# Optimization experiments

Hardware: AMD Instinct MI355X
Metric: run time of the kernel (lower is better)

## Reference

```python
import jax, jax.numpy as jnp
import numpy as np

B, OBS, ACT_DIM, C, CTX, H = 128, 512, 7, 100, 128, 512
IN = OBS + 1 + CTX  # states + scalar action component + context = 641


def cont2disc(values, n):
    return jnp.clip(jnp.floor((values + 1.0) / 2.0 * n), 0, n - 1)


def setup_inputs() -> dict:
    key = jax.random.key(0)
    ks = jax.random.split(key, 10)
    def w(k, shape):
        return jax.random.normal(k, shape, dtype=jnp.float32) / np.sqrt(shape[-2])
    return {
        "observations": jax.random.normal(ks[0], (B, OBS), dtype=jnp.float32),
        "actions": jax.random.uniform(ks[1], (B, ACT_DIM), dtype=jnp.float32, minval=-1.0, maxval=1.0),
        # one MLP per action dim (weight_sharing=False): layers IN->H->H->CTX
        "W1": w(ks[2], (ACT_DIM, IN, H)),  "b1": jnp.zeros((ACT_DIM, H), jnp.float32),
        "W2": w(ks[3], (ACT_DIM, H, H)),   "b2": jnp.zeros((ACT_DIM, H), jnp.float32),
        "W3": w(ks[4], (ACT_DIM, H, CTX)), "b3": jnp.zeros((ACT_DIM, CTX), jnp.float32),
        # output_proj = MLP((1,)): single dense CTX->1, no activation
        "Wp": w(ks[5], (CTX, 1)), "bp": jnp.zeros((1,), jnp.float32),
        "compute_lse": 1,
    }


def reference(observations, actions, W1, b1, W2, b2, W3, b3, Wp, bp, compute_lse):
    n = observations.shape[0]
    acts = cont2disc(actions, C)  # [B, ACT_DIM], float component indices
    context = jnp.zeros((n, CTX), observations.dtype)
    comp = jnp.arange(C, dtype=observations.dtype)  # candidate components 0..C-1
    q = jnp.zeros((n, ACT_DIM * C), observations.dtype)

    for i in range(1, ACT_DIM):
        def mlp(x, i=i):  # hidden layers relu, final layer linear
            h = jax.nn.relu(x @ W1[i] + b1[i])
            h = jax.nn.relu(h @ W2[i] + b2[i])
            return h @ W3[i] + b3[i]

        # batched over all num_components candidate actions (replaces the per-j loop)
        xin = jnp.concatenate([
            jnp.broadcast_to(observations[:, None, :], (n, C, OBS)),
            jnp.broadcast_to(comp[None, :, None], (n, C, 1)),
            jnp.broadcast_to(context[:, None, :], (n, C, CTX)),
        ], axis=-1)  # [B, C, IN]
        curr_ctx = mlp(xin) + context[:, None, :]        # [B, C, CTX]
        qv = (curr_ctx @ Wp + bp)[..., 0]                # [B, C]
        q = q.at[:, (i - 1) * C : i * C].set(qv)          # which_qval ordering

        # advance context with the actual (discretized) action
        x = jnp.concatenate([observations, acts[:, i:i + 1], context], axis=-1)
        context = mlp(x) + context

    if compute_lse:
        return jax.scipy.special.logsumexp(q, axis=-1)    # [B]
    return context @ Wp + bp                              # [B, 1]
```

## Files before the change

### kernel.cpp

```cpp
#include <hip/hip_runtime.h>
#include <math.h>

#define BATCH 128
#define ACT 7
#define NC 100
#define CTXD 128
#define HID 512
#define QW 600

typedef __attribute__((ext_vector_type(8))) __bf16 bf16x8;
typedef __attribute__((ext_vector_type(4))) float f32x4;
typedef __attribute__((ext_vector_type(4))) unsigned short u16x4;

__device__ __forceinline__ unsigned short f2bf(float f) {
    union { float f; unsigned int u; } v; v.f = f;
    unsigned int u = v.u;
    return (unsigned short)((u + 0x7fffu + ((u >> 16) & 1u)) >> 16);
}
__device__ __forceinline__ unsigned int pack2bf(float a, float b) {
    unsigned int ua = __float_as_uint(a) + 0x8000u;
    unsigned int ub = __float_as_uint(b) + 0x8000u;
    return (ua >> 16) | (ub & 0xffff0000u);
}

__device__ __forceinline__ void async16(const void* g, void* l) {
    __builtin_amdgcn_global_load_lds(
        (const __attribute__((address_space(1))) unsigned int*)(uintptr_t)g,
        (__attribute__((address_space(3))) unsigned int*)(unsigned int)(uintptr_t)l,
        16, 0, 0);
}

__global__ void cvt_kernel(const float* __restrict__ obs, const float* __restrict__ W1,
                           const float* __restrict__ W2, const float* __restrict__ W3,
                           unsigned short* __restrict__ obs_bf, unsigned short* __restrict__ W1Cbf,
                           unsigned short* __restrict__ W2bf, unsigned short* __restrict__ W3bf) {
    const int e = (blockIdx.x * 256 + threadIdx.x) * 4;
    const float* src; unsigned short* dst;
    if (e < 65536)        { src = obs + e; dst = obs_bf + e; }
    else if (e < 458752)  { int f = e - 65536; int i = f >> 16; int rem = f & 65535;
                            src = W1 + (size_t)(i + 1) * 328192 + 513*512 + rem; dst = W1Cbf + f; }
    else if (e < 2031616) { int f = e - 458752; src = W2 + 262144 + f; dst = W2bf + f; }
    else                  { int f = e - 2031616; src = W3 + 65536 + f; dst = W3bf + f; }
    float4 v = *(const float4*)src;
    u16x4 o; o[0] = f2bf(v.x); o[1] = f2bf(v.y); o[2] = f2bf(v.z); o[3] = f2bf(v.w);
    *(u16x4*)dst = o;
}

__global__ void prep_transpose(const float* __restrict__ W1, const float* __restrict__ W2,
                               unsigned short* __restrict__ W1AT, unsigned short* __restrict__ W2T) {
    __shared__ float tile[32][33];
    const int z = blockIdx.z;
    const float* ip; unsigned short* op;
    if (z < 6) { ip = W1 + (size_t)(z + 1) * 328192; op = W1AT + (size_t)z * 262144; }
    else       { int i = z - 6; ip = W2 + (size_t)(i + 1) * 262144; op = W2T + (size_t)i * 262144; }
    const int r0 = blockIdx.x * 32, c0 = blockIdx.y * 32;
    const int tx = threadIdx.x, ty = threadIdx.y;
    #pragma unroll
    for (int j = 0; j < 32; j += 8)
        tile[ty + j][tx] = ip[(size_t)(r0 + ty + j) * 512 + c0 + tx];
    __syncthreads();
    #pragma unroll
    for (int j = 0; j < 32; j += 8)
        op[(size_t)(c0 + ty + j) * 512 + r0 + tx] = f2bf(tile[tx][ty + j]);
}

__global__ void vq_kernel(const float* __restrict__ W3, const float* __restrict__ Wp,
                          float* __restrict__ vq) {
    const int z = blockIdx.x, k = threadIdx.x;
    const float4* row = (const float4*)(W3 + (size_t)(z + 1) * 65536 + (size_t)k * 128);
    const float4* wp4 = (const float4*)Wp;
    float s = 0.f;
    #pragma unroll 8
    for (int n = 0; n < 32; ++n) {
        float4 a = row[n], w = wp4[n];
        s += a.x*w.x + a.y*w.y + a.z*w.z + a.w*w.w;
    }
    vq[z * 512 + k] = s;
}

__launch_bounds__(256)
__global__ void yobs_kernel(const unsigned short* __restrict__ A,
                            const unsigned short* __restrict__ BtAll,
                            const float* __restrict__ b1,
                            float* __restrict__ Yobs) {
    __shared__ unsigned short As[64*32];
    __shared__ unsigned short Bs[128*32];
    const int m0 = blockIdx.x * 64;
    const int n0 = blockIdx.y * 128;
    const int z  = blockIdx.z;
    const unsigned short* Bt = BtAll + (size_t)z * 262144;
    const int tid = threadIdx.x, lane = tid & 63, wave = tid >> 6;
    const int wm = wave >> 1, wn = wave & 1;
    const int srow = tid >> 2, skc = (tid & 3) * 8;
    const unsigned short* gA  = A  + (size_t)(m0 + srow) * HID + skc;
    const unsigned short* gB0 = Bt + (size_t)(n0 + srow) * HID + skc;
    const unsigned short* gB1 = gB0 + 64 * HID;
    f32x4 acc[2][4] = {};
    for (int k0 = 0; k0 < HID; k0 += 32) {
        async16(gA + k0, As + tid*8);
        async16(gB0 + k0, Bs + tid*8);
        async16(gB1 + k0, Bs + 2048 + tid*8);
        __syncthreads();
        const int q8 = (lane >> 4) * 8, l15 = lane & 15;
        bf16x8 af[2], bfr[4];
        #pragma unroll
        for (int mt = 0; mt < 2; ++mt)
            af[mt] = *(const bf16x8*)(As + (wm*32 + mt*16 + l15) * 32 + q8);
        #pragma unroll
        for (int nt = 0; nt < 4; ++nt)
            bfr[nt] = *(const bf16x8*)(Bs + (wn*64 + nt*16 + l15) * 32 + q8);
        #pragma unroll
        for (int mt = 0; mt < 2; ++mt)
            #pragma unroll
            for (int nt = 0; nt < 4; ++nt)
                acc[mt][nt] = __builtin_amdgcn_mfma_f32_16x16x32_bf16(af[mt], bfr[nt], acc[mt][nt], 0, 0, 0);
        __syncthreads();
    }
    const int colL = wn*64 + (lane & 15);
    #pragma unroll
    for (int nt = 0; nt < 4; ++nt) {
        const int col = n0 + colL + nt*16;
        const float bb = b1[(z + 1) * HID + col];
        #pragma unroll
        for (int mt = 0; mt < 2; ++mt)
            #pragma unroll
            for (int r = 0; r < 4; ++r) {
                const int row = m0 + wm*32 + mt*16 + (lane >> 4)*4 + r;
                Yobs[(size_t)z * 65536 + (size_t)row * HID + col] = acc[mt][nt][r] + bb;
            }
    }
}

__launch_bounds__(1024)
__global__ void chain_kernel(const float* __restrict__ Yobs, const float* __restrict__ W1,
                             const unsigned short* __restrict__ W1Cbf,
                             const unsigned short* __restrict__ W2bf,
                             const unsigned short* __restrict__ W3bf,
                             const float* __restrict__ b2, const float* __restrict__ b3,
                             const float* __restrict__ actions,
                             const float* __restrict__ Wp, const float* __restrict__ bp,
                             float* __restrict__ Y0all, float* __restrict__ QOFF) {
    const int b = blockIdx.x, t = threadIdx.x;
    __shared__ float ctx[128], h1[512], h2s[512];
    __shared__ float part[2048];
    const int pair = t & 255, kq = t >> 8;
    const int pair3 = t & 63, kq3 = t >> 6;
    if (t < 128) ctx[t] = 0.f;
    __syncthreads();
    for (int i = 1; i <= 6; ++i) {
        if (t < 128) part[t] = (ctx[t] + b3[i*128 + t]) * Wp[t];
        __syncthreads();
        if (t < 64) {
            float v = part[t] + part[t + 64];
            #pragma unroll
            for (int o = 32; o > 0; o >>= 1) v += __shfl_down(v, o, 64);
            if (t == 0) QOFF[(i-1)*128 + b] = v + bp[0];
        }
        __syncthreads();
        const float a = actions[b*ACT + i];
        float fj = floorf((a + 1.0f) * 50.0f);
        fj = fminf(fmaxf(fj, 0.0f), 99.0f);
        {
            const unsigned int* wp1 = (const unsigned int*)(W1Cbf + (size_t)(i-1)*65536) + pair;
            float acc0 = 0.f, acc1 = 0.f;
            #pragma unroll 8
            for (int k = kq*32; k < kq*32 + 32; ++k) {
                unsigned int u = wp1[k*256];
                float c = ctx[k];
                acc0 = fmaf(c, __uint_as_float(u << 16), acc0);
                acc1 = fmaf(c, __uint_as_float(u & 0xffff0000u), acc1);
            }
            *(float2*)(&part[kq*512 + 2*pair]) = make_float2(acc0, acc1);
        }
        __syncthreads();
        if (t < 256) {
            const int n2 = 2*t;
            float2 p0 = *(const float2*)(&part[n2]);
            float2 p1 = *(const float2*)(&part[512 + n2]);
            float2 p2 = *(const float2*)(&part[1024 + n2]);
            float2 p3 = *(const float2*)(&part[1536 + n2]);
            float2 yo = *(const float2*)(Yobs + (size_t)(i-1)*65536 + b*512 + n2);
            float y0a = yo.x + p0.x + p1.x + p2.x + p3.x;
            float y0b = yo.y + p0.y + p1.y + p2.y + p3.y;
            *(float2*)(Y0all + (size_t)(i-1)*65536 + b*512 + n2) = make_float2(y0a, y0b);
            const float* w1a = W1 + (size_t)i*328192 + 262144;
            float2 wv = *(const float2*)(w1a + n2);
            h1[n2]   = fmaxf(fmaf(fj, wv.x, y0a), 0.f);
            h1[n2+1] = fmaxf(fmaf(fj, wv.y, y0b), 0.f);
        }
        __syncthreads();
        {
            const unsigned int* wp2 = (const unsigned int*)(W2bf + (size_t)(i-1)*262144) + pair;
            float acc0 = 0.f, acc1 = 0.f;
            #pragma unroll 16
            for (int k = kq*128; k < kq*128 + 128; ++k) {
                unsigned int u = wp2[k*256];
                float hv = h1[k];
                acc0 = fmaf(hv, __uint_as_float(u << 16), acc0);
                acc1 = fmaf(hv, __uint_as_float(u & 0xffff0000u), acc1);
            }
            *(float2*)(&part[kq*512 + 2*pair]) = make_float2(acc0, acc1);
        }
        __syncthreads();
        if (t < 256) {
            const int n2 = 2*t;
            float2 p0 = *(const float2*)(&part[n2]);
            float2 p1 = *(const float2*)(&part[512 + n2]);
            float2 p2 = *(const float2*)(&part[1024 + n2]);
            float2 p3 = *(const float2*)(&part[1536 + n2]);
            float2 bb = *(const float2*)(b2 + i*512 + n2);
            h2s[n2]   = fmaxf(p0.x + p1.x + p2.x + p3.x + bb.x, 0.f);
            h2s[n2+1] = fmaxf(p0.y + p1.y + p2.y + p3.y + bb.y, 0.f);
        }
        __syncthreads();
        {
            const unsigned int* wp3 = (const unsigned int*)(W3bf + (size_t)(i-1)*65536) + pair3;
            float acc0 = 0.f, acc1 = 0.f;
            #pragma unroll 8
            for (int k = kq3*32; k < kq3*32 + 32; ++k) {
                unsigned int u = wp3[k*64];
                float hv = h2s[k];
                acc0 = fmaf(hv, __uint_as_float(u << 16), acc0);
                acc1 = fmaf(hv, __uint_as_float(u & 0xffff0000u), acc1);
            }
            *(float2*)(&part[kq3*128 + 2*pair3]) = make_float2(acc0, acc1);
        }
        __syncthreads();
        if (t < 128) {
            float s = 0.f;
            #pragma unroll
            for (int qg = 0; qg < 16; ++qg) s += part[qg*128 + t];
            ctx[t] = s + b3[i*128 + t] + ctx[t];
        }
        __syncthreads();
    }
}

__launch_bounds__(256)
__global__ void h2all_kernel(const float* __restrict__ Y0all, const float* __restrict__ W1,
                             const unsigned short* __restrict__ W2T, const float* __restrict__ b2,
                             const float* __restrict__ vq, float* __restrict__ qpart) {
    __shared__ unsigned short As[2][4096];
    __shared__ unsigned short Bs[2][4096];
    const int bx = blockIdx.x;
    const int z  = bx / 100;
    const int r0 = bx * 128;
    const int r2 = (bx % 100) * 128;
    const int n0 = blockIdx.y * 128;
    const int tid = threadIdx.x, lane = tid & 63, wave = tid >> 6;
    const int wm = wave >> 1, wn = wave & 1;
    const int srow = tid >> 2, skc = (tid & 3) * 8;
    const int l15 = lane & 15, q8 = (lane >> 4) * 8;
    const int rA = srow, kc = skc;
    const int rowg1 = r2 + rA, rowg2 = r2 + rA + 64;
    const float c1 = (float)(rowg1 % 100), c2 = (float)(rowg2 % 100);
    const float* y1p = Y0all + (size_t)z*65536 + (size_t)(rowg1/100)*512;
    const float* y2p = Y0all + (size_t)z*65536 + (size_t)(rowg2/100)*512;
    const float* w1a = W1 + (size_t)(z+1)*328192 + 262144;
    const unsigned short* gB0 = W2T + (size_t)z*262144 + (size_t)(n0 + srow)*512 + skc;
    const unsigned short* gB1 = gB0 + 64*512;
    f32x4 acc[4][4] = {};
    for (int k0 = 0; k0 < 512; k0 += 64) {
        #pragma unroll
        for (int h = 0; h < 2; ++h) {
            const int k = k0 + h*32 + kc;
            float4 wv0 = *(const float4*)(w1a + k);
            float4 wv1 = *(const float4*)(w1a + k + 4);
            float4 ya0 = *(const float4*)(y1p + k);
            float4 ya1 = *(const float4*)(y1p + k + 4);
            float4 yb0 = *(const float4*)(y2p + k);
            float4 yb1 = *(const float4*)(y2p + k + 4);
            uint4 o;
            o.x = pack2bf(fmaxf(fmaf(c1, wv0.x, ya0.x), 0.f), fmaxf(fmaf(c1, wv0.y, ya0.y), 0.f));
            o.y = pack2bf(fmaxf(fmaf(c1, wv0.z, ya0.z), 0.f), fmaxf(fmaf(c1, wv0.w, ya0.w), 0.f));
            o.z = pack2bf(fmaxf(fmaf(c1, wv1.x, ya1.x), 0.f), fmaxf(fmaf(c1, wv1.y, ya1.y), 0.f));
            o.w = pack2bf(fmaxf(fmaf(c1, wv1.z, ya1.z), 0.f), fmaxf(fmaf(c1, wv1.w, ya1.w), 0.f));
            *(uint4*)(&As[h][rA*32 + kc]) = o;
            o.x = pack2bf(fmaxf(fmaf(c2, wv0.x, yb0.x), 0.f), fmaxf(fmaf(c2, wv0.y, yb0.y), 0.f));
            o.y = pack2bf(fmaxf(fmaf(c2, wv0.z, yb0.z), 0.f), fmaxf(fmaf(c2, wv0.w, yb0.w), 0.f));
            o.z = pack2bf(fmaxf(fmaf(c2, wv1.x, yb1.x), 0.f), fmaxf(fmaf(c2, wv1.y, yb1.y), 0.f));
            o.w = pack2bf(fmaxf(fmaf(c2, wv1.z, yb1.z), 0.f), fmaxf(fmaf(c2, wv1.w, yb1.w), 0.f));
            *(uint4*)(&As[h][(rA + 64)*32 + kc]) = o;
        }
        async16(gB0 + k0,      &Bs[0][tid*8]);
        async16(gB1 + k0,      &Bs[0][2048 + tid*8]);
        async16(gB0 + k0 + 32, &Bs[1][tid*8]);
        async16(gB1 + k0 + 32, &Bs[1][2048 + tid*8]);
        __syncthreads();
        #pragma unroll
        for (int h = 0; h < 2; ++h) {
            bf16x8 af[4], bfr[4];
            #pragma unroll
            for (int mt = 0; mt < 4; ++mt)
                af[mt] = *(const bf16x8*)(&As[h][(wm*64 + mt*16 + l15)*32 + q8]);
            #pragma unroll
            for (int nt = 0; nt < 4; ++nt)
                bfr[nt] = *(const bf16x8*)(&Bs[h][(wn*64 + nt*16 + l15)*32 + q8]);
            #pragma unroll
            for (int mt = 0; mt < 4; ++mt)
                #pragma unroll
                for (int nt = 0; nt < 4; ++nt)
                    acc[mt][nt] = __builtin_amdgcn_mfma_f32_16x16x32_bf16(af[mt], bfr[nt], acc[mt][nt], 0, 0, 0);
        }
        __syncthreads();
    }
    float vb[4], bb[4];
    #pragma unroll
    for (int nt = 0; nt < 4; ++nt) {
        const int col = n0 + wn*64 + nt*16 + l15;
        bb[nt] = b2[(z+1)*512 + col];
        vb[nt] = vq[z*512 + col];
    }
    const int plane = blockIdx.y * 2 + wn;
    const int gq = lane >> 4;
    #pragma unroll
    for (int mt = 0; mt < 4; ++mt)
        #pragma unroll
        for (int r = 0; r < 4; ++r) {
            float p = 0.f;
            #pragma unroll
            for (int nt = 0; nt < 4; ++nt)
                p = fmaf(fmaxf(acc[mt][nt][r] + bb[nt], 0.f), vb[nt], p);
            p += __shfl_xor(p, 1, 64);
            p += __shfl_xor(p, 2, 64);
            p += __shfl_xor(p, 4, 64);
            p += __shfl_xor(p, 8, 64);
            if (l15 == 0) {
                const int grow = r0 + wm*64 + mt*16 + gq*4 + r;
                qpart[(size_t)plane * 76800 + grow] = p;
            }
        }
}

__global__ void lse_kernel(const float* __restrict__ qpart, const float* __restrict__ QOFF,
                           float* __restrict__ out) {
    __shared__ float red[256];
    __shared__ float qs[QW];
    const int b = blockIdx.x, t = threadIdx.x;
    for (int k = t; k < QW; k += 256) {
        const int z = k / 100, gc = k - z * 100;
        const int grow = z * 12800 + b * 100 + gc;
        float s = QOFF[z * 128 + b];
        #pragma unroll
        for (int p = 0; p < 8; ++p) s += qpart[(size_t)p * 76800 + grow];
        qs[k] = s;
    }
    __syncthreads();
    float m = 0.0f;
    for (int k = t; k < QW; k += 256) m = fmaxf(m, qs[k]);
    red[t] = m; __syncthreads();
    for (int s = 128; s > 0; s >>= 1) { if (t < s) red[t] = fmaxf(red[t], red[t+s]); __syncthreads(); }
    m = red[0]; __syncthreads();
    float sum = 0.0f;
    for (int k = t; k < QW; k += 256) sum += expf(qs[k] - m);
    red[t] = sum; __syncthreads();
    for (int s = 128; s > 0; s >>= 1) { if (t < s) red[t] += red[t+s]; __syncthreads(); }
    if (t == 0) out[b] = logf(red[0] + 100.0f * expf(-m)) + m;
}

extern "C" void kernel_launch(void* const* d_in, const int* in_sizes, int n_in,
                              void* d_out, int out_size, void* d_ws, size_t ws_size,
                              hipStream_t stream) {
    const float* obs     = (const float*)d_in[0];
    const float* actions = (const float*)d_in[1];
    const float* W1      = (const float*)d_in[2];
    const float* b1      = (const float*)d_in[3];
    const float* W2      = (const float*)d_in[4];
    const float* b2      = (const float*)d_in[5];
    const float* W3      = (const float*)d_in[6];
    const float* b3      = (const float*)d_in[7];
    const float* Wp      = (const float*)d_in[8];
    const float* bp      = (const float*)d_in[9];
    float* out = (float*)d_out;
    float* ws  = (float*)d_ws;

    unsigned short* obs_bf = (unsigned short*)(ws);
    unsigned short* W1AT   = (unsigned short*)(ws + 32768);
    unsigned short* W2T    = (unsigned short*)(ws + 819200);
    unsigned short* W1Cbf  = (unsigned short*)(ws + 1605632);
    unsigned short* W2bf   = (unsigned short*)(ws + 1802240);
    unsigned short* W3bf   = (unsigned short*)(ws + 2588672);
    float* Yobs  = ws + 2785280;
    float* Y0all = ws + 3178496;
    float* QOFF  = ws + 3571712;
    float* vq    = ws + 3572736;
    float* qpart = ws + 3575808;

    cvt_kernel<<<2368, 256, 0, stream>>>(obs, W1, W2, W3, obs_bf, W1Cbf, W2bf, W3bf);
    prep_transpose<<<dim3(16,16,12), dim3(32,8), 0, stream>>>(W1, W2, W1AT, W2T);
    vq_kernel<<<6, 512, 0, stream>>>(W3, Wp, vq);
    yobs_kernel<<<dim3(2,4,6), 256, 0, stream>>>(obs_bf, W1AT, b1, Yobs);
    chain_kernel<<<BATCH, 1024, 0, stream>>>(Yobs, W1, W1Cbf, W2bf, W3bf, b2, b3, actions, Wp, bp, Y0all, QOFF);
    h2all_kernel<<<dim3(600, 4), 256, 0, stream>>>(Y0all, W1, W2T, b2, vq, qpart);
    lse_kernel<<<BATCH, 256, 0, stream>>>(qpart, QOFF, out);
}
```

Before: 243.4 us.

## Split fused H1 build out of layer-2 GEMM into separate bf16 materialization kernel

Replaces the GEMM that recomputed relu(Y0 + c*W1col) into shared memory in every block with a separate elementwise kernel that writes H1 as bf16 to global memory. The GEMM then loads both A and B tiles via async copies. The grid is also swapped so the four column planes sharing a row tile run adjacently, improving L2 reuse of H1. This removes the redundant per-block fp32 loads and conversion work (each A row was rebuilt for four column blocks), at the cost of an extra launch and a roughly 78 MB bf16 write plus read.

New measurement: 248.6 us. +2.1%, slower.

```diff
diff --git a/kernel.cpp b/kernel.cpp
--- a/kernel.cpp
+++ b/kernel.cpp
@@ -236,52 +236,51 @@
     }
 }
 
+__global__ void h1all_kernel(const float* __restrict__ Y0all, const float* __restrict__ W1,
+                             unsigned short* __restrict__ H1) {
+    const int t = blockIdx.x * 256 + threadIdx.x;
+    const int row = t >> 6, kc = (t & 63) << 3;
+    const int z = row / 12800, rr = row - z * 12800;
+    const int b = rr / 100;
+    const float c = (float)(rr - b * 100);
+    const float* yp = Y0all + (size_t)z*65536 + (size_t)b*512 + kc;
+    const float* wp = W1 + (size_t)(z+1)*328192 + 262144 + kc;
+    float4 ya = *(const float4*)(yp), yb = *(const float4*)(yp + 4);
+    float4 wa = *(const float4*)(wp), wb = *(const float4*)(wp + 4);
+    uint4 o;
+    o.x = pack2bf(fmaxf(fmaf(c, wa.x, ya.x), 0.f), fmaxf(fmaf(c, wa.y, ya.y), 0.f));
+    o.y = pack2bf(fmaxf(fmaf(c, wa.z, ya.z), 0.f), fmaxf(fmaf(c, wa.w, ya.w), 0.f));
+    o.z = pack2bf(fmaxf(fmaf(c, wb.x, yb.x), 0.f), fmaxf(fmaf(c, wb.y, yb.y), 0.f));
+    o.w = pack2bf(fmaxf(fmaf(c, wb.z, yb.z), 0.f), fmaxf(fmaf(c, wb.w, yb.w), 0.f));
+    *(uint4*)(H1 + (size_t)row * 512 + kc) = o;
+}
+
 __launch_bounds__(256)
-__global__ void h2all_kernel(const float* __restrict__ Y0all, const float* __restrict__ W1,
-                             const unsigned short* __restrict__ W2T, const float* __restrict__ b2,
-                             const float* __restrict__ vq, float* __restrict__ qpart) {
+__global__ void gemm2q_kernel(const unsigned short* __restrict__ H1,
+                              const unsigned short* __restrict__ W2T,
+                              const float* __restrict__ b2,
+                              const float* __restrict__ vq, float* __restrict__ qpart) {
     __shared__ unsigned short As[2][4096];
     __shared__ unsigned short Bs[2][4096];
-    const int bx = blockIdx.x;
-    const int z  = bx / 100;
-    const int r0 = bx * 128;
-    const int r2 = (bx % 100) * 128;
-    const int n0 = blockIdx.y * 128;
+    const int plane = blockIdx.x;
+    const int rt = blockIdx.y;
+    const int z  = rt / 100;
+    const int r0 = rt * 128;
+    const int n0 = plane * 128;
     const int tid = threadIdx.x, lane = tid & 63, wave = tid >> 6;
     const int wm = wave >> 1, wn = wave & 1;
     const int srow = tid >> 2, skc = (tid & 3) * 8;
     const int l15 = lane & 15, q8 = (lane >> 4) * 8;
-    const int rA = srow, kc = skc;
-    const int rowg1 = r2 + rA, rowg2 = r2 + rA + 64;
-    const float c1 = (float)(rowg1 % 100), c2 = (float)(rowg2 % 100);
-    const float* y1p = Y0all + (size_t)z*65536 + (size_t)(rowg1/100)*512;
-    const float* y2p = Y0all + (size_t)z*65536 + (size_t)(rowg2/100)*512;
-    const float* w1a = W1 + (size_t)(z+1)*328192 + 262144;
+    const unsigned short* gA0 = H1 + (size_t)(r0 + srow)*512 + skc;
+    const unsigned short* gA1 = gA0 + 64*512;
     const unsigned short* gB0 = W2T + (size_t)z*262144 + (size_t)(n0 + srow)*512 + skc;
     const unsigned short* gB1 = gB0 + 64*512;
     f32x4 acc[4][4] = {};
     for (int k0 = 0; k0 < 512; k0 += 64) {
-        #pragma unroll
-        for (int h = 0; h < 2; ++h) {
-            const int k = k0 + h*32 + kc;
-            float4 wv0 = *(const float4*)(w1a + k);
-            float4 wv1 = *(const float4*)(w1a + k + 4);
-            float4 ya0 = *(const float4*)(y1p + k);
-            float4 ya1 = *(const float4*)(y1p + k + 4);
-            float4 yb0 = *(const float4*)(y2p + k);
-            float4 yb1 = *(const float4*)(y2p + k + 4);
-            uint4 o;
-            o.x = pack2bf(fmaxf(fmaf(c1, wv0.x, ya0.x), 0.f), fmaxf(fmaf(c1, wv0.y, ya0.y), 0.f));
-            o.y = pack2bf(fmaxf(fmaf(c1, wv0.z, ya0.z), 0.f), fmaxf(fmaf(c1, wv0.w, ya0.w), 0.f));
-            o.z = pack2bf(fmaxf(fmaf(c1, wv1.x, ya1.x), 0.f), fmaxf(fmaf(c1, wv1.y, ya1.y), 0.f));
-            o.w = pack2bf(fmaxf(fmaf(c1, wv1.z, ya1.z), 0.f), fmaxf(fmaf(c1, wv1.w, ya1.w), 0.f));
-            *(uint4*)(&As[h][rA*32 + kc]) = o;
-            o.x = pack2bf(fmaxf(fmaf(c2, wv0.x, yb0.x), 0.f), fmaxf(fmaf(c2, wv0.y, yb0.y), 0.f));
-            o.y = pack2bf(fmaxf(fmaf(c2, wv0.z, yb0.z), 0.f), fmaxf(fmaf(c2, wv0.w, yb0.w), 0.f));
-            o.z = pack2bf(fmaxf(fmaf(c2, wv1.x, yb1.x), 0.f), fmaxf(fmaf(c2, wv1.y, yb1.y), 0.f));
-            o.w = pack2bf(fmaxf(fmaf(c2, wv1.z, yb1.z), 0.f), fmaxf(fmaf(c2, wv1.w, yb1.w), 0.f));
-            *(uint4*)(&As[h][(rA + 64)*32 + kc]) = o;
-        }
+        async16(gA0 + k0,      &As[0][tid*8]);
+        async16(gA1 + k0,      &As[0][2048 + tid*8]);
+        async16(gA0 + k0 + 32, &As[1][tid*8]);
+        async16(gA1 + k0 + 32, &As[1][2048 + tid*8]);
         async16(gB0 + k0,      &Bs[0][tid*8]);
         async16(gB1 + k0,      &Bs[0][2048 + tid*8]);
         async16(gB0 + k0 + 32, &Bs[1][tid*8]);
@@ -311,7 +310,7 @@
         bb[nt] = b2[(z+1)*512 + col];
         vb[nt] = vq[z*512 + col];
     }
-    const int plane = blockIdx.y * 2 + wn;
+    const int plane2 = plane * 2 + wn;
     const int gq = lane >> 4;
     #pragma unroll
     for (int mt = 0; mt < 4; ++mt)
@@ -327,7 +326,7 @@
             p += __shfl_xor(p, 8, 64);
             if (l15 == 0) {
                 const int grow = r0 + wm*64 + mt*16 + gq*4 + r;
-                qpart[(size_t)plane * 76800 + grow] = p;
+                qpart[(size_t)plane2 * 76800 + grow] = p;
             }
         }
 }
@@ -385,12 +384,14 @@
     float* QOFF  = ws + 3571712;
     float* vq    = ws + 3572736;
     float* qpart = ws + 3575808;
+    unsigned short* H1 = (unsigned short*)(ws + 4190208);
 
     cvt_kernel<<<2368, 256, 0, stream>>>(obs, W1, W2, W3, obs_bf, W1Cbf, W2bf, W3bf);
     prep_transpose<<<dim3(16,16,12), dim3(32,8), 0, stream>>>(W1, W2, W1AT, W2T);
     vq_kernel<<<6, 512, 0, stream>>>(W3, Wp, vq);
     yobs_kernel<<<dim3(2,4,6), 256, 0, stream>>>(obs_bf, W1AT, b1, Yobs);
     chain_kernel<<<BATCH, 1024, 0, stream>>>(Yobs, W1, W1Cbf, W2bf, W3bf, b2, b3, actions, Wp, bp, Y0all, QOFF);
-    h2all_kernel<<<dim3(600, 4), 256, 0, stream>>>(Y0all, W1, W2T, b2, vq, qpart);
+    h1all_kernel<<<19200, 256, 0, stream>>>(Y0all, W1, H1);
+    gemm2q_kernel<<<dim3(4, 600), 256, 0, stream>>>(H1, W2T, b2, vq, qpart);
     lse_kernel<<<BATCH, 256, 0, stream>>>(qpart, QOFF, out);
 }
```
